# Kernel optimization log

Measured on AMD Instinct MI355X. Metric: run time of the kernel, lower is better.

## Reference

```python
import jax, jax.numpy as jnp
import numpy as np

N_WIRES = 3  # state vector of 2^3 = 8 amplitudes, kept as [B,2,2,2]


def _rx(t):
    c = jnp.cos(t / 2); s = jnp.sin(t / 2)
    return jnp.stack([jnp.stack([c + 0j, -1j * s], -1),
                      jnp.stack([-1j * s, c + 0j], -1)], -2).astype(jnp.complex64)


def _ry(t):
    c = jnp.cos(t / 2); s = jnp.sin(t / 2)
    return jnp.stack([jnp.stack([c, -s], -1),
                      jnp.stack([s, c], -1)], -2).astype(jnp.complex64)


def _rz(t):
    e = jnp.exp(-1j * t / 2).astype(jnp.complex64)
    z = jnp.zeros_like(e)
    return jnp.stack([jnp.stack([e, z], -1),
                      jnp.stack([z, jnp.conj(e)], -1)], -2)


def apply_1q(state, mat, wire):
    # state: [B,2,2,2]; mat: [2,2] (shared) or [B,2,2] (per-sample)
    s = jnp.moveaxis(state, 1 + wire, 1)
    sh = s.shape
    s = s.reshape(sh[0], 2, -1)
    m = jnp.broadcast_to(mat, (sh[0], 2, 2))
    s = jnp.einsum('bij,bjk->bik', m, s)
    return jnp.moveaxis(s.reshape(sh), 1, 1 + wire)


def apply_crx(state, t, ctrl, tgt):
    # controlled-RX: apply rx(t) to target subspace where control bit == 1
    mat = _rx(t)  # [2,2]
    s = jnp.moveaxis(state, (1 + ctrl, 1 + tgt), (1, 2))  # [B,2(ctrl),2(tgt),2]
    s1 = s[:, 1]                       # [B,2,2]
    sh = s1.shape
    s1 = jnp.einsum('ij,bjk->bik', mat, s1.reshape(sh[0], 2, -1)).reshape(sh)
    s = jnp.stack([s[:, 0], s1], 1)
    return jnp.moveaxis(s, (1, 2), (1 + ctrl, 1 + tgt))


def _quantum_forward(x, theta, W1, b1, W2, b2):
    B = x.shape[0]
    state = jnp.zeros((B, 2, 2, 2), jnp.complex64).at[:, 0, 0, 0].set(1.0)
    # GeneralEncoder: rx(x0)@w0, ry(x1)@w1, rz(x2)@w2
    state = apply_1q(state, _rx(x[:, 0]), 0)
    state = apply_1q(state, _ry(x[:, 1]), 1)
    state = apply_1q(state, _rz(x[:, 2]), 2)
    # RandomLayer(n_ops=8): fixed representative 8-op trainable sequence
    state = apply_1q(state, _rx(theta[0]), 0)
    state = apply_1q(state, _ry(theta[1]), 1)
    state = apply_1q(state, _rz(theta[2]), 2)
    state = apply_crx(state, theta[3], 0, 1)
    state = apply_1q(state, _ry(theta[4]), 2)
    state = apply_1q(state, _rx(theta[5]), 1)
    state = apply_crx(state, theta[6], 1, 2)
    state = apply_1q(state, _rz(theta[7]), 0)
    # measurement -> 8 basis-state probabilities (matches Linear(8,32) head)
    probs = (state.real ** 2 + state.imag ** 2).reshape(B, 8)
    h = jax.nn.relu(probs @ W1 + b1)
    return h @ W2 + b2


def setup_inputs() -> dict:
    key = jax.random.key(0)
    ks = jax.random.split(key, 6)
    B = 2_000_000
    x = jax.random.normal(ks[0], (B, 3), jnp.float32)
    theta = jax.random.normal(ks[1], (8,), jnp.float32)
    W1 = jax.random.normal(ks[2], (8, 32), jnp.float32) * 0.35   # ~1/sqrt(8)
    b1 = jnp.zeros((32,), jnp.float32)
    W2 = jax.random.normal(ks[3], (32, 2), jnp.float32) * 0.18   # ~1/sqrt(32)
    b2 = jnp.zeros((2,), jnp.float32)
    return {"x": x, "theta": theta, "W1": W1, "b1": b1, "W2": W2, "b2": b2}


def reference(x, theta, W1, b1, W2, b2):
    return _quantum_forward(x, theta, W1, b1, W2, b2)
```

## Files before the change

kernel.cpp:

```cpp
#include <hip/hip_runtime.h>

__global__ __launch_bounds__(256) void q_fused(
    const float* __restrict__ x,
    const float* __restrict__ theta,
    const float* __restrict__ W1,
    const float* __restrict__ b1,
    const float* __restrict__ W2,
    const float* __restrict__ b2,
    float* __restrict__ out,
    int B)
{
    __shared__ float Ure[8][8];
    __shared__ float Uim[8][8];
    __shared__ float4 lt4[98];

    const int lid  = threadIdx.x;
    const int t    = blockIdx.x * 256 + lid;
    const int base = t * 8;

    if (lid < 8) {
        float cr[8], ci[8];
        #pragma unroll
        for (int r = 0; r < 8; ++r) { cr[r] = (r == lid) ? 1.f : 0.f; ci[r] = 0.f; }

        auto rxmix = [&](int a, int b, float c_, float s_) {
            float ar = cr[a], ai = ci[a], br = cr[b], bi = ci[b];
            cr[a] = c_*ar + s_*bi;   ci[a] = c_*ai - s_*br;
            cr[b] = s_*ai + c_*br;   ci[b] = -s_*ar + c_*bi;
        };
        auto rymix = [&](int a, int b, float c_, float s_) {
            float ar = cr[a], ai = ci[a], br = cr[b], bi = ci[b];
            cr[a] = c_*ar - s_*br;   ci[a] = c_*ai - s_*bi;
            cr[b] = s_*ar + c_*br;   ci[b] = s_*ai + c_*bi;
        };
        auto zmul = [&](int r, float u, float v) {
            float xr = cr[r], xi = ci[r];
            cr[r] = xr*u - xi*v;  ci[r] = xr*v + xi*u;
        };

        float c, s;
        __sincosf(theta[0]*0.5f, &s, &c);
        rxmix(0,4,c,s); rxmix(1,5,c,s); rxmix(2,6,c,s); rxmix(3,7,c,s);
        __sincosf(theta[1]*0.5f, &s, &c);
        rymix(0,2,c,s); rymix(1,3,c,s); rymix(4,6,c,s); rymix(5,7,c,s);
        __sincosf(theta[2]*0.5f, &s, &c);
        #pragma unroll
        for (int r = 0; r < 8; ++r) zmul(r, c, (r & 1) ? s : -s);
        __sincosf(theta[3]*0.5f, &s, &c);
        rxmix(4,6,c,s); rxmix(5,7,c,s);
        __sincosf(theta[4]*0.5f, &s, &c);
        rymix(0,1,c,s); rymix(2,3,c,s); rymix(4,5,c,s); rymix(6,7,c,s);
        __sincosf(theta[5]*0.5f, &s, &c);
        rxmix(0,2,c,s); rxmix(1,3,c,s); rxmix(4,6,c,s); rxmix(5,7,c,s);
        __sincosf(theta[6]*0.5f, &s, &c);
        rxmix(2,3,c,s); rxmix(6,7,c,s);
        __sincosf(theta[7]*0.5f, &s, &c);
        #pragma unroll
        for (int r = 0; r < 8; ++r) zmul(r, c, (r < 4) ? -s : s);

        #pragma unroll
        for (int r = 0; r < 8; ++r) { Ure[r][lid] = cr[r]; Uim[r][lid] = ci[r]; }
    }
    __syncthreads();

    if (lid < 32) {
        float Wre[8][4], Wim[8][4];
        #pragma unroll
        for (int j = 0; j < 8; ++j) {
            Wre[j][0] =  Ure[j][0]; Wim[j][0] =  Uim[j][0];
            Wre[j][1] =  Ure[j][2]; Wim[j][1] =  Uim[j][2];
            Wre[j][2] =  Uim[j][4]; Wim[j][2] = -Ure[j][4];
            Wre[j][3] =  Uim[j][6]; Wim[j][3] = -Ure[j][6];
        }
        float Q[4][4];
        #pragma unroll
        for (int m = 0; m < 4; ++m)
            #pragma unroll
            for (int n = 0; n < 4; ++n) Q[m][n] = 0.f;
        #pragma unroll
        for (int j = 0; j < 8; ++j) {
            float w = W1[j*32 + lid];
            #pragma unroll
            for (int m = 0; m < 4; ++m)
                #pragma unroll
                for (int n = 0; n < 4; ++n)
                    Q[m][n] = fmaf(w, Wre[j][m]*Wre[j][n] + Wim[j][m]*Wim[j][n], Q[m][n]);
        }
        float R[3][3];
        R[0][0] = Q[0][0];
        R[0][1] = Q[0][1] + Q[1][0];
        R[0][2] = Q[1][1];
        R[1][0] = Q[0][2] + Q[2][0];
        R[1][1] = Q[0][3] + Q[1][2] + Q[2][1] + Q[3][0];
        R[1][2] = Q[1][3] + Q[3][1];
        R[2][0] = Q[2][2];
        R[2][1] = Q[2][3] + Q[3][2];
        R[2][2] = Q[3][3];
        float P[3][3];
        #pragma unroll
        for (int b = 0; b < 3; ++b) {
            P[0][b] = 0.5f*(R[0][b] + R[2][b]);
            P[1][b] = 0.5f*(R[0][b] - R[2][b]);
            P[2][b] = 0.5f*R[1][b];
        }
        float T[3][3];
        #pragma unroll
        for (int si = 0; si < 3; ++si) {
            T[si][0] = 0.5f*(P[si][0] + P[si][2]);
            T[si][1] = 0.5f*(P[si][0] - P[si][2]);
            T[si][2] = 0.5f*P[si][1];
        }
        float* row = ((float*)lt4) + lid*12;
        row[0] = T[0][1]; row[1] = T[0][2]; row[2] = T[1][0]; row[3] = T[2][0];
        row[4] = T[1][1]; row[5] = T[1][2]; row[6] = T[2][1]; row[7] = T[2][2];
        row[8] = b1[lid] + T[0][0];
        row[9]  = W2[lid*2+0];
        row[10] = W2[lid*2+1];
        row[11] = 0.f;
    }
    if (lid == 0) {
        float* f = (float*)lt4;
        f[384] = b2[0]; f[385] = b2[1]; f[386] = 0.f; f[387] = 0.f;
        f[388] = 0.f;   f[389] = 0.f;   f[390] = 0.f; f[391] = 0.f;
    }
    __syncthreads();

    const float* ltf = (const float*)lt4;
    const float b2a = ltf[384], b2b = ltf[385];

    if (base + 8 <= B) {
        float4 xa[6];
        const float4* X4 = (const float4*)x;
        #pragma unroll
        for (int i = 0; i < 6; ++i) xa[i] = X4[t*6 + i];

        const float* xf = (const float*)xa;
        float C0[8], S0[8], C1[8], S1[8], Pcc[8], Pcs[8], Psc[8], Pss[8];
        #pragma unroll
        for (int k = 0; k < 8; ++k) {
            __sincosf(xf[3*k+0], &S0[k], &C0[k]);
            __sincosf(xf[3*k+1], &S1[k], &C1[k]);
            Pcc[k] = C0[k]*C1[k]; Pcs[k] = C0[k]*S1[k];
            Psc[k] = S0[k]*C1[k]; Pss[k] = S0[k]*S1[k];
        }
        float acc0[8], acc1[8];
        #pragma unroll
        for (int k = 0; k < 8; ++k) { acc0[k] = b2a; acc1[k] = b2b; }

        #pragma unroll 1
        for (int l = 0; l < 32; ++l) {
            float4 cA = lt4[l*3+0];
            float4 cB = lt4[l*3+1];
            float4 cC = lt4[l*3+2];
            #pragma unroll
            for (int k = 0; k < 8; ++k) {
                float h = cC.x;
                h = fmaf(cA.x, C1[k],  h);
                h = fmaf(cA.y, S1[k],  h);
                h = fmaf(cA.z, C0[k],  h);
                h = fmaf(cA.w, S0[k],  h);
                h = fmaf(cB.x, Pcc[k], h);
                h = fmaf(cB.y, Pcs[k], h);
                h = fmaf(cB.z, Psc[k], h);
                h = fmaf(cB.w, Pss[k], h);
                h = fmaxf(h, 0.f);
                acc0[k] = fmaf(h, cC.y, acc0[k]);
                acc1[k] = fmaf(h, cC.z, acc1[k]);
            }
        }
        float4* O4 = (float4*)out;
        #pragma unroll
        for (int k = 0; k < 4; ++k)
            O4[t*4+k] = make_float4(acc0[2*k], acc1[2*k], acc0[2*k+1], acc1[2*k+1]);
    } else if (base < B) {
        for (int e = base; e < B; ++e) {
            float s0, c0, s1, c1;
            __sincosf(x[e*3+0], &s0, &c0);
            __sincosf(x[e*3+1], &s1, &c1);
            float pcc = c0*c1, pcs = c0*s1, psc = s0*c1, pss = s0*s1;
            float A0 = b2a, A1 = b2b;
            for (int l = 0; l < 32; ++l) {
                const float* row = ltf + l*12;
                float h = row[8];
                h = fmaf(row[0], c1,  h);
                h = fmaf(row[1], s1,  h);
                h = fmaf(row[2], c0,  h);
                h = fmaf(row[3], s0,  h);
                h = fmaf(row[4], pcc, h);
                h = fmaf(row[5], pcs, h);
                h = fmaf(row[6], psc, h);
                h = fmaf(row[7], pss, h);
                h = fmaxf(h, 0.f);
                A0 = fmaf(h, row[9],  A0);
                A1 = fmaf(h, row[10], A1);
            }
            out[e*2+0] = A0;
            out[e*2+1] = A1;
        }
    }
}

extern "C" void kernel_launch(void* const* d_in, const int* in_sizes, int n_in,
                              void* d_out, int out_size, void* d_ws, size_t ws_size,
                              hipStream_t stream) {
    const float* x     = (const float*)d_in[0];
    const float* theta = (const float*)d_in[1];
    const float* W1    = (const float*)d_in[2];
    const float* b1    = (const float*)d_in[3];
    const float* W2    = (const float*)d_in[4];
    const float* b2    = (const float*)d_in[5];
    float* out = (float*)d_out;

    const int B = in_sizes[0] / 3;
    const int nT = (B + 7) / 8;
    const int blocks = (nT + 255) / 256;
    q_fused<<<blocks, 256, 0, stream>>>(x, theta, W1, b1, W2, b2, out, B);
}
```

Measured before the change: 116.5 us.

## Split table precompute into separate kernel and use hardware sin/cos builtins

Moves the per-block unitary and lookup-table construction into a one-block precompute kernel that writes the table to workspace. The main kernel then reads the table from global memory as uniform loads instead of rebuilding it in shared memory with two barriers per block. The sin/cos calls are replaced with the AMD hardware sin/cos builtins on inputs pre-scaled by 1/(2π), and the hidden-unit loop is unrolled by two. The cost is an extra kernel launch and table reads through the cache, and the hardware transcendental may lose accuracy for large arguments.

```diff
diff --git a/kernel.cpp b/kernel.cpp
--- a/kernel.cpp
+++ b/kernel.cpp
@@ -1,27 +1,22 @@
 #include <hip/hip_runtime.h>
 
-__global__ __launch_bounds__(256) void q_fused(
-    const float* __restrict__ x,
+
+__global__ __launch_bounds__(64) void q_precompute(
     const float* __restrict__ theta,
     const float* __restrict__ W1,
     const float* __restrict__ b1,
     const float* __restrict__ W2,
     const float* __restrict__ b2,
-    float* __restrict__ out,
-    int B)
+    float* __restrict__ tab)
 {
     __shared__ float Ure[8][8];
     __shared__ float Uim[8][8];
-    __shared__ float4 lt4[98];
-
-    const int lid  = threadIdx.x;
-    const int t    = blockIdx.x * 256 + lid;
-    const int base = t * 8;
-
-    if (lid < 8) {
+    const int t = threadIdx.x;
+
+    if (t < 8) {
         float cr[8], ci[8];
         #pragma unroll
-        for (int r = 0; r < 8; ++r) { cr[r] = (r == lid) ? 1.f : 0.f; ci[r] = 0.f; }
+        for (int r = 0; r < 8; ++r) { cr[r] = (r == t) ? 1.f : 0.f; ci[r] = 0.f; }
 
         auto rxmix = [&](int a, int b, float c_, float s_) {
             float ar = cr[a], ai = ci[a], br = cr[b], bi = ci[b];
@@ -59,11 +54,11 @@
         for (int r = 0; r < 8; ++r) zmul(r, c, (r < 4) ? -s : s);
 
         #pragma unroll
-        for (int r = 0; r < 8; ++r) { Ure[r][lid] = cr[r]; Uim[r][lid] = ci[r]; }
+        for (int r = 0; r < 8; ++r) { Ure[r][t] = cr[r]; Uim[r][t] = ci[r]; }
     }
     __syncthreads();
 
-    if (lid < 32) {
+    if (t < 32) {
         float Wre[8][4], Wim[8][4];
         #pragma unroll
         for (int j = 0; j < 8; ++j) {
@@ -79,7 +74,7 @@
             for (int n = 0; n < 4; ++n) Q[m][n] = 0.f;
         #pragma unroll
         for (int j = 0; j < 8; ++j) {
-            float w = W1[j*32 + lid];
+            float w = W1[j*32 + t];
             #pragma unroll
             for (int m = 0; m < 4; ++m)
                 #pragma unroll
@@ -110,23 +105,30 @@
             T[si][1] = 0.5f*(P[si][0] - P[si][2]);
             T[si][2] = 0.5f*P[si][1];
         }
-        float* row = ((float*)lt4) + lid*12;
+        float* row = tab + t*12;
         row[0] = T[0][1]; row[1] = T[0][2]; row[2] = T[1][0]; row[3] = T[2][0];
         row[4] = T[1][1]; row[5] = T[1][2]; row[6] = T[2][1]; row[7] = T[2][2];
-        row[8] = b1[lid] + T[0][0];
-        row[9]  = W2[lid*2+0];
-        row[10] = W2[lid*2+1];
+        row[8] = b1[t] + T[0][0];
+        row[9]  = W2[t*2+0];
+        row[10] = W2[t*2+1];
         row[11] = 0.f;
     }
-    if (lid == 0) {
-        float* f = (float*)lt4;
-        f[384] = b2[0]; f[385] = b2[1]; f[386] = 0.f; f[387] = 0.f;
-        f[388] = 0.f;   f[389] = 0.f;   f[390] = 0.f; f[391] = 0.f;
-    }
-    __syncthreads();
-
-    const float* ltf = (const float*)lt4;
-    const float b2a = ltf[384], b2b = ltf[385];
+    if (t == 0) { tab[384] = b2[0]; tab[385] = b2[1]; tab[386] = 0.f; tab[387] = 0.f; }
+}
+
+#define INV_2PI 0.15915494309189535f
+
+__global__ __launch_bounds__(256) void q_main(
+    const float* __restrict__ x,
+    const float* __restrict__ tab,
+    float* __restrict__ out,
+    int B)
+{
+    const int t    = blockIdx.x * 256 + threadIdx.x;
+    const int base = t * 8;
+    if (base >= B) return;
+
+    const float b2a = tab[384], b2b = tab[385];
 
     if (base + 8 <= B) {
         float4 xa[6];
@@ -138,8 +140,12 @@
         float C0[8], S0[8], C1[8], S1[8], Pcc[8], Pcs[8], Psc[8], Pss[8];
         #pragma unroll
         for (int k = 0; k < 8; ++k) {
-            __sincosf(xf[3*k+0], &S0[k], &C0[k]);
-            __sincosf(xf[3*k+1], &S1[k], &C1[k]);
+            float r0 = xf[3*k+0] * INV_2PI;
+            float r1 = xf[3*k+1] * INV_2PI;
+            S0[k] = __builtin_amdgcn_sinf(r0);
+            C0[k] = __builtin_amdgcn_cosf(r0);
+            S1[k] = __builtin_amdgcn_sinf(r1);
+            C1[k] = __builtin_amdgcn_cosf(r1);
             Pcc[k] = C0[k]*C1[k]; Pcs[k] = C0[k]*S1[k];
             Psc[k] = S0[k]*C1[k]; Pss[k] = S0[k]*S1[k];
         }
@@ -147,11 +153,12 @@
         #pragma unroll
         for (int k = 0; k < 8; ++k) { acc0[k] = b2a; acc1[k] = b2b; }
 
-        #pragma unroll 1
+        const float4* T4 = (const float4*)tab;
+        #pragma unroll 2
         for (int l = 0; l < 32; ++l) {
-            float4 cA = lt4[l*3+0];
-            float4 cB = lt4[l*3+1];
-            float4 cC = lt4[l*3+2];
+            float4 cA = T4[l*3+0];
+            float4 cB = T4[l*3+1];
+            float4 cC = T4[l*3+2];
             #pragma unroll
             for (int k = 0; k < 8; ++k) {
                 float h = cC.x;
@@ -172,15 +179,17 @@
         #pragma unroll
         for (int k = 0; k < 4; ++k)
             O4[t*4+k] = make_float4(acc0[2*k], acc1[2*k], acc0[2*k+1], acc1[2*k+1]);
-    } else if (base < B) {
+    } else {
         for (int e = base; e < B; ++e) {
             float s0, c0, s1, c1;
-            __sincosf(x[e*3+0], &s0, &c0);
-            __sincosf(x[e*3+1], &s1, &c1);
+            float r0 = x[e*3+0] * INV_2PI;
+            float r1 = x[e*3+1] * INV_2PI;
+            s0 = __builtin_amdgcn_sinf(r0); c0 = __builtin_amdgcn_cosf(r0);
+            s1 = __builtin_amdgcn_sinf(r1); c1 = __builtin_amdgcn_cosf(r1);
             float pcc = c0*c1, pcs = c0*s1, psc = s0*c1, pss = s0*s1;
             float A0 = b2a, A1 = b2b;
             for (int l = 0; l < 32; ++l) {
-                const float* row = ltf + l*12;
+                const float* row = tab + l*12;
                 float h = row[8];
                 h = fmaf(row[0], c1,  h);
                 h = fmaf(row[1], s1,  h);
@@ -210,9 +219,13 @@
     const float* W2    = (const float*)d_in[4];
     const float* b2    = (const float*)d_in[5];
     float* out = (float*)d_out;
+    float* tab = (float*)d_ws;
 
     const int B = in_sizes[0] / 3;
+
+    q_precompute<<<1, 64, 0, stream>>>(theta, W1, b1, W2, b2, tab);
+
     const int nT = (B + 7) / 8;
     const int blocks = (nT + 255) / 256;
-    q_fused<<<blocks, 256, 0, stream>>>(x, theta, W1, b1, W2, b2, out, B);
+    q_main<<<blocks, 256, 0, stream>>>(x, tab, out, B);
 }
```

After: 101.7 us. 1.15x faster.
